# Performance work log

Hardware: AMD Instinct MI355X
Metric: run time of the kernel (lower is better)

Reference implementation:

```python
import jax, jax.numpy as jnp
import numpy as np

N, C_IN, C_OUT, T, V = 32, 4, 64, 6, 512


def setup_inputs() -> dict:
    key = jax.random.key(0)
    ks = jax.random.split(key, 8)
    x = jax.random.normal(ks[0], (N, C_IN, T, V), dtype=jnp.float32)
    # A carries 7 (unused) adjacency channels + 1 binary mask channel
    A = jax.random.randint(ks[1], (N, 8, V, V), 0, 2, dtype=jnp.int32)
    conv_w = jax.random.normal(ks[2], (C_OUT, C_IN), dtype=jnp.float32) / np.sqrt(C_IN).astype(np.float32)
    conv_b = jax.random.normal(ks[3], (C_OUT,), dtype=jnp.float32) * 0.02
    l2_w = jax.random.normal(ks[4], (1, T), dtype=jnp.float32) / np.sqrt(T).astype(np.float32)
    l2_b = jax.random.normal(ks[5], (1,), dtype=jnp.float32) * 0.02
    l1_w = jax.random.normal(ks[6], (1, 2 * C_OUT), dtype=jnp.float32) / np.sqrt(2 * C_OUT).astype(np.float32)
    l1_b = jax.random.normal(ks[7], (1,), dtype=jnp.float32) * 0.02
    return {"x": x, "A": A, "conv_w": conv_w, "conv_b": conv_b,
            "l2_w": l2_w, "l2_b": l2_b, "l1_w": l1_w, "l1_b": l1_b}


def reference(x, A, conv_w, conv_b, l2_w, l2_b, l1_w, l1_b):
    c = conv_w.shape[0]
    # 1x1 conv over (t, v): pure channel mix
    xc = jnp.einsum('nctv,oc->notv', x, conv_w) + conv_b[None, :, None, None]  # (n, 64, t, v)
    # temporal squeeze via l2: Linear(6 -> 1) on last (t) axis
    x1 = jnp.einsum('nctv,t->nvc', xc, l2_w[0]) + l2_b[0]  # (n, v, 64)
    # GAT-style pairwise score: l1(cat(x1_i, x1_j)) decomposes into two rank-1 terms
    e_i = x1 @ l1_w[0, :c]   # (n, v)
    e_j = x1 @ l1_w[0, c:]   # (n, v)
    scores = e_i[:, :, None] + e_j[:, None, :] + l1_b[0]  # (n, v, v), [n,i,j]
    scores = jnp.where(scores >= 0, scores, 0.2 * scores)  # LeakyReLU(0.2)
    # mask channel: A[:,7]; mask.long()==0 -> -inf
    mask = A[:, 7]  # (n, v, v) int
    scores = jnp.where(mask == 0, -jnp.inf, scores)
    p = jax.nn.softmax(scores, axis=2)
    p = jnp.where(jnp.isnan(p), 0.0, p)  # fully-masked rows -> 0
    # aggregate: nctv,ndvw->nctw with d=1
    out = jnp.einsum('nctv,nvw->nctw', xc, p)
    return out, p[:, None]  # (n, 64, t, v), (n, 1, v, v)
```

## Files before the change

### kernel.cpp

```cpp
#include <hip/hip_runtime.h>
#include <hip/hip_bf16.h>
#include <math.h>

#define NB   32
#define CIN  4
#define COUT 64
#define TT   6
#define VV   512
#define P_OFF (NB*COUT*TT*VV)
#define SPLITS 8
#define CH   (VV/SPLITS)
#define NROW 24
#define E_FLOATS (2*NB*VV)
#define PKW  516

typedef __attribute__((ext_vector_type(8))) short bf16x8;
typedef __attribute__((ext_vector_type(4))) float f32x4;

__device__ inline unsigned int pack2(float a, float b) {
    __hip_bfloat162 h = __float22bfloat162_rn(make_float2(a, b));
    return *reinterpret_cast<unsigned int*>(&h);
}

__global__ __launch_bounds__(256) void e_kernel(
    const float* __restrict__ x,
    const float* __restrict__ conv_w,
    const float* __restrict__ conv_b,
    const float* __restrict__ l2_w,
    const float* __restrict__ l2_b,
    const float* __restrict__ l1_w,
    float* __restrict__ e)
{
    __shared__ float W1[CIN], W2[CIN], cst[2];
    int tid = threadIdx.x;
    if (tid < CIN) {
        float w1 = 0.f, w2 = 0.f;
        for (int o = 0; o < COUT; ++o) {
            w1 += l1_w[o]        * conv_w[o*CIN + tid];
            w2 += l1_w[COUT + o] * conv_w[o*CIN + tid];
        }
        W1[tid] = w1; W2[tid] = w2;
    }
    if (tid == CIN) {
        float B1 = 0.f, B2 = 0.f, S1 = 0.f, S2 = 0.f;
        for (int o = 0; o < COUT; ++o) {
            B1 += l1_w[o]        * conv_b[o];
            B2 += l1_w[COUT + o] * conv_b[o];
            S1 += l1_w[o];
            S2 += l1_w[COUT + o];
        }
        float Ls = 0.f;
        for (int t = 0; t < TT; ++t) Ls += l2_w[t];
        cst[0] = Ls*B1 + l2_b[0]*S1;
        cst[1] = Ls*B2 + l2_b[0]*S2;
    }
    __syncthreads();

    int idx = blockIdx.x * 256 + tid;
    int n = idx >> 9, v = idx & (VV-1);
    float ei = cst[0], ej = cst[1];
    #pragma unroll
    for (int c = 0; c < CIN; ++c) {
        float wc1 = W1[c], wc2 = W2[c];
        #pragma unroll
        for (int t = 0; t < TT; ++t) {
            float xv = x[((n*CIN + c)*TT + t)*VV + v];
            float lw = l2_w[t];
            ei += lw*wc1*xv;
            ej += lw*wc2*xv;
        }
    }
    e[idx]         = ei;
    e[NB*VV + idx] = ej;
}

__global__ __launch_bounds__(512, 4) void fused_kernel(
    const float* __restrict__ x,
    const int*   __restrict__ A,
    const float* __restrict__ e,
    const float* __restrict__ l1_b,
    float*       __restrict__ p,
    float*       __restrict__ ypart)
{
    __shared__ float xst[CH][33];
    __shared__ unsigned int pk[16][PKW];

    int s = blockIdx.x;
    int n = blockIdx.y;
    int tid = threadIdx.x;
    int lane = tid & 63;
    int q = tid >> 6;

    for (int idx = tid; idx < CH*33; idx += 512) {
        int r = idx >> 6;
        int i = idx & 63;
        float v = 0.f;
        if (r < NROW)       v = x[((size_t)n*NROW + r)*VV + s*CH + i];
        else if (r == NROW) v = 1.f;
        xst[i][r] = v;
    }

    float l1b_val = l1_b[0];
    float4 ej0 = *(const float4*)(e + NB*VV + n*VV + lane*8);
    float4 ej1 = *(const float4*)(e + NB*VV + n*VV + lane*8 + 4);
    float ejv[8] = {ej0.x, ej0.y, ej0.z, ej0.w, ej1.x, ej1.y, ej1.z, ej1.w};

    const int* mbase = A + (size_t)(n*8 + 7)*VV*VV;

    f32x4 acc[2][4];
    #pragma unroll
    for (int mt = 0; mt < 2; ++mt)
        #pragma unroll
        for (int t = 0; t < 4; ++t) acc[mt][t] = (f32x4){0.f, 0.f, 0.f, 0.f};

    bf16x8 afr[2][2];

    int4 mA0, mA1, mB0, mB1;
    float bA, bB;
    {
        int i0 = s*CH + q*2;
        const int* mr = mbase + (size_t)i0*VV + lane*8;
        mA0 = *(const int4*)mr;       mA1 = *(const int4*)(mr + 4);
        mB0 = *(const int4*)(mr+VV);  mB1 = *(const int4*)(mr + VV + 4);
        bA = e[n*VV + i0]; bB = e[n*VV + i0 + 1];
    }

    for (int sub = 0; sub < 4; ++sub) {
        int i_gA = s*CH + sub*16 + q*2;

        int4 cA0 = mA0, cA1 = mA1, cB0 = mB0, cB1 = mB1;
        float biasA = bA + l1b_val, biasB = bB + l1b_val;

        if (sub < 3) {
            const int* mr = mbase + (size_t)(i_gA + 16)*VV + lane*8;
            mA0 = *(const int4*)mr;       mA1 = *(const int4*)(mr + 4);
            mB0 = *(const int4*)(mr+VV);  mB1 = *(const int4*)(mr + VV + 4);
            bA = e[n*VV + i_gA + 16]; bB = e[n*VV + i_gA + 17];
        }

        float svA[8], svB[8];
        int mkA[8] = {cA0.x,cA0.y,cA0.z,cA0.w, cA1.x,cA1.y,cA1.z,cA1.w};
        int mkB[8] = {cB0.x,cB0.y,cB0.z,cB0.w, cB1.x,cB1.y,cB1.z,cB1.w};
        #pragma unroll
        for (int m2 = 0; m2 < 8; ++m2) {
            float tA = biasA + ejv[m2]; tA = (tA >= 0.f) ? tA : 0.2f*tA;
            svA[m2] = (mkA[m2] == 0) ? -INFINITY : tA;
            float tB = biasB + ejv[m2]; tB = (tB >= 0.f) ? tB : 0.2f*tB;
            svB[m2] = (mkB[m2] == 0) ? -INFINITY : tB;
        }
        float mA = svA[0], mB = svB[0];
        #pragma unroll
        for (int m2 = 1; m2 < 8; ++m2) {
            mA = fmaxf(mA, svA[m2]); mB = fmaxf(mB, svB[m2]);
        }
        #pragma unroll
        for (int off = 32; off; off >>= 1) {
            mA = fmaxf(mA, __shfl_xor(mA, off));
            mB = fmaxf(mB, __shfl_xor(mB, off));
        }
        float sumA = 0.f, sumB = 0.f;
        if (mA > -INFINITY) {
            #pragma unroll
            for (int m2 = 0; m2 < 8; ++m2) { svA[m2] = __expf(svA[m2]-mA); sumA += svA[m2]; }
        } else {
            #pragma unroll
            for (int m2 = 0; m2 < 8; ++m2) svA[m2] = 0.f;
        }
        if (mB > -INFINITY) {
            #pragma unroll
            for (int m2 = 0; m2 < 8; ++m2) { svB[m2] = __expf(svB[m2]-mB); sumB += svB[m2]; }
        } else {
            #pragma unroll
            for (int m2 = 0; m2 < 8; ++m2) svB[m2] = 0.f;
        }
        #pragma unroll
        for (int off = 32; off; off >>= 1) {
            sumA += __shfl_xor(sumA, off);
            sumB += __shfl_xor(sumB, off);
        }
        float invA = (sumA > 0.f) ? 1.f/sumA : 0.f;
        float invB = (sumB > 0.f) ? 1.f/sumB : 0.f;
        #pragma unroll
        for (int m2 = 0; m2 < 8; ++m2) { svA[m2] *= invA; svB[m2] *= invB; }

        float* prA = p + ((size_t)(n*VV + i_gA))*VV + lane*8;
        float4 pA03 = {svA[0],svA[1],svA[2],svA[3]}, pA47 = {svA[4],svA[5],svA[6],svA[7]};
        float4 pB03 = {svB[0],svB[1],svB[2],svB[3]}, pB47 = {svB[4],svB[5],svB[6],svB[7]};
        *(float4*)prA            = pA03;
        *(float4*)(prA + 4)      = pA47;
        *(float4*)(prA + VV)     = pB03;
        *(float4*)(prA + VV + 4) = pB47;

        {
            int pr = (sub & 1)*8 + q;
            uint4 u0 = {pack2(svA[0],svB[0]), pack2(svA[1],svB[1]),
                        pack2(svA[2],svB[2]), pack2(svA[3],svB[3])};
            uint4 u1 = {pack2(svA[4],svB[4]), pack2(svA[5],svB[5]),
                        pack2(svA[6],svB[6]), pack2(svA[7],svB[7])};
            *(uint4*)&pk[pr][lane*8]     = u0;
            *(uint4*)&pk[pr][lane*8 + 4] = u1;
        }

        if (sub & 1) {
            __syncthreads();

            if (sub == 1) {
                #pragma unroll
                for (int g = 0; g < 2; ++g)
                    #pragma unroll
                    for (int mt = 0; mt < 2; ++mt) {
                        int r  = mt*16 + (lane & 15);
                        int kb = g*32 + (lane >> 4)*8;
                        union { unsigned int u[4]; bf16x8 v; } ua;
                        #pragma unroll
                        for (int t = 0; t < 4; ++t)
                            ua.u[t] = pack2(xst[kb + 2*t][r], xst[kb + 2*t + 1][r]);
                        afr[g][mt] = ua.v;
                    }
            }

            int g = sub >> 1;
            #pragma unroll
            for (int t = 0; t < 4; ++t) {
                int ncol = (q*4 + t)*16 + (lane & 15);
                union { unsigned int u[4]; bf16x8 v; } ub;
                #pragma unroll
                for (int jj = 0; jj < 4; ++jj)
                    ub.u[jj] = pk[(lane >> 4)*4 + jj][ncol];
                acc[0][t] = __builtin_amdgcn_mfma_f32_16x16x32_bf16(afr[g][0], ub.v, acc[0][t], 0, 0, 0);
                acc[1][t] = __builtin_amdgcn_mfma_f32_16x16x32_bf16(afr[g][1], ub.v, acc[1][t], 0, 0, 0);
            }
            if (sub == 1) __syncthreads();
        }
    }

    float* yo = ypart + (size_t)(s*NB + n)*25*VV;
    #pragma unroll
    for (int mt = 0; mt < 2; ++mt)
        #pragma unroll
        for (int t = 0; t < 4; ++t) {
            int ncol = (q*4 + t)*16 + (lane & 15);
            #pragma unroll
            for (int reg = 0; reg < 4; ++reg) {
                int row = mt*16 + (lane >> 4)*4 + reg;
                if (row < 25)
                    yo[(size_t)row*VV + ncol] = acc[mt][t][reg];
            }
        }
}

__global__ __launch_bounds__(256) void expand_kernel(
    const float* __restrict__ ypart,
    const float* __restrict__ conv_w,
    const float* __restrict__ conv_b,
    float*       __restrict__ out)
{
    __shared__ float ysm[25][64];
    __shared__ float wsm[COUT*CIN];
    __shared__ float bsm[COUT];

    int wc = blockIdx.x;
    int n  = blockIdx.y;
    int tid = threadIdx.x;

    if (tid < COUT*CIN) wsm[tid] = conv_w[tid];
    if (tid < COUT)     bsm[tid] = conv_b[tid];

    for (int l4 = tid; l4 < 400; l4 += 256) {
        int r = l4 >> 4, w4 = l4 & 15;
        float4 a = {0.f, 0.f, 0.f, 0.f};
        #pragma unroll
        for (int s = 0; s < SPLITS; ++s) {
            float4 v = *(const float4*)(ypart +
                ((size_t)(s*NB + n)*25 + r)*VV + wc*64 + w4*4);
            a.x += v.x; a.y += v.y; a.z += v.z; a.w += v.w;
        }
        *(float4*)&ysm[r][w4*4] = a;
    }
    __syncthreads();

    int w  = tid & 63;
    int og = tid >> 6;

    float y[25];
    #pragma unroll
    for (int r = 0; r < 25; ++r) y[r] = ysm[r][w];

    #pragma unroll
    for (int oo = 0; oo < 16; ++oo) {
        int o = og*16 + oo;
        float wb[CIN];
        #pragma unroll
        for (int c = 0; c < CIN; ++c) wb[c] = wsm[o*CIN + c];
        float bo = bsm[o];
        #pragma unroll
        for (int t = 0; t < TT; ++t) {
            float val = bo * y[24];
            #pragma unroll
            for (int c = 0; c < CIN; ++c) val = fmaf(wb[c], y[c*TT + t], val);
            out[((size_t)(n*COUT + o)*TT + t)*VV + wc*64 + w] = val;
        }
    }
}

extern "C" void kernel_launch(void* const* d_in, const int* in_sizes, int n_in,
                              void* d_out, int out_size, void* d_ws, size_t ws_size,
                              hipStream_t stream)
{
    const float* x      = (const float*)d_in[0];
    const int*   A      = (const int*)  d_in[1];
    const float* conv_w = (const float*)d_in[2];
    const float* conv_b = (const float*)d_in[3];
    const float* l2_w   = (const float*)d_in[4];
    const float* l2_b   = (const float*)d_in[5];
    const float* l1_w   = (const float*)d_in[6];
    const float* l1_b   = (const float*)d_in[7];

    float* out = (float*)d_out;
    float* pP  = out + P_OFF;
    float* e   = (float*)d_ws;
    float* yp  = e + E_FLOATS;

    e_kernel<<<NB*VV/256, 256, 0, stream>>>(x, conv_w, conv_b, l2_w, l2_b, l1_w, e);

    dim3 gf(SPLITS, NB);
    fused_kernel<<<gf, 512, 0, stream>>>(x, A, e, l1_b, pP, yp);

    dim3 ge(8, NB);
    expand_kernel<<<ge, 256, 0, stream>>>(yp, conv_w, conv_b, out);
}
```

Baseline: 34.62 us.

## Pre-pack mask channel into a bitmask in a wide prep kernel

A new prep pass, launched as thousands of extra blocks of the e-computation kernel, reads the int32 mask channel and packs it into one bit per entry in workspace. The fused softmax/aggregation kernel then stages its slice of the bitmask and the e_i values in shared memory instead of streaming int32 mask rows with register prefetch. The aim is to move the bandwidth-heavy mask read into a kernel with far more parallelism, away from the latency-bound fused kernel. The cost is an extra workspace write and read, plus one more __syncthreads in the fused kernel.

```diff
diff --git a/kernel.cpp b/kernel.cpp
--- a/kernel.cpp
+++ b/kernel.cpp
@@ -12,7 +12,9 @@
 #define CH   (VV/SPLITS)
 #define NROW 24
 #define E_FLOATS (2*NB*VV)
+#define BM_U32 (NB*VV*16)
 #define PKW  516
+#define MPK_BLOCKS 4096
 
 typedef __attribute__((ext_vector_type(8))) short bf16x8;
 typedef __attribute__((ext_vector_type(4))) float f32x4;
@@ -22,17 +24,38 @@
     return *reinterpret_cast<unsigned int*>(&h);
 }
 
-__global__ __launch_bounds__(256) void e_kernel(
+__global__ __launch_bounds__(256) void prep_kernel(
     const float* __restrict__ x,
+    const int*   __restrict__ A,
     const float* __restrict__ conv_w,
     const float* __restrict__ conv_b,
     const float* __restrict__ l2_w,
     const float* __restrict__ l2_b,
     const float* __restrict__ l1_w,
-    float* __restrict__ e)
+    float* __restrict__ e,
+    unsigned char* __restrict__ bm)
 {
     __shared__ float W1[CIN], W2[CIN], cst[2];
     int tid = threadIdx.x;
+    int b   = blockIdx.x;
+
+    if (b < MPK_BLOCKS) {
+        size_t t  = (size_t)b*256 + tid;
+        int nr    = (int)(t >> 6);
+        int byt   = (int)(t & 63);
+        int n     = nr >> 9, i = nr & 511;
+        const int* src = A + (((size_t)(n*8 + 7)*VV + i)*VV) + byt*8;
+        int4 a0 = *(const int4*)src;
+        int4 a1 = *(const int4*)(src + 4);
+        unsigned int byte =
+            (unsigned)(a0.x != 0)       | ((unsigned)(a0.y != 0) << 1) |
+            ((unsigned)(a0.z != 0) << 2) | ((unsigned)(a0.w != 0) << 3) |
+            ((unsigned)(a1.x != 0) << 4) | ((unsigned)(a1.y != 0) << 5) |
+            ((unsigned)(a1.z != 0) << 6) | ((unsigned)(a1.w != 0) << 7);
+        bm[(size_t)nr*64 + byt] = (unsigned char)byte;
+        return;
+    }
+
     if (tid < CIN) {
         float w1 = 0.f, w2 = 0.f;
         for (int o = 0; o < COUT; ++o) {
@@ -56,7 +79,7 @@
     }
     __syncthreads();
 
-    int idx = blockIdx.x * 256 + tid;
+    int idx = (b - MPK_BLOCKS) * 256 + tid;
     int n = idx >> 9, v = idx & (VV-1);
     float ei = cst[0], ej = cst[1];
     #pragma unroll
@@ -76,7 +99,7 @@
 
 __global__ __launch_bounds__(512, 4) void fused_kernel(
     const float* __restrict__ x,
-    const int*   __restrict__ A,
+    const unsigned int* __restrict__ bm32,
     const float* __restrict__ e,
     const float* __restrict__ l1_b,
     float*       __restrict__ p,
@@ -84,6 +107,8 @@
 {
     __shared__ float xst[CH][33];
     __shared__ unsigned int pk[16][PKW];
+    __shared__ unsigned int mlds[CH][16];
+    __shared__ float eld[CH];
 
     int s = blockIdx.x;
     int n = blockIdx.y;
@@ -99,14 +124,17 @@
         else if (r == NROW) v = 1.f;
         xst[i][r] = v;
     }
+    for (int l = tid; l < CH*16; l += 512) {
+        int il = l >> 4, d = l & 15;
+        mlds[il][d] = bm32[((size_t)n*VV + s*CH + il)*16 + d];
+    }
+    if (tid < CH) eld[tid] = e[n*VV + s*CH + tid];
 
     float l1b_val = l1_b[0];
     float4 ej0 = *(const float4*)(e + NB*VV + n*VV + lane*8);
     float4 ej1 = *(const float4*)(e + NB*VV + n*VV + lane*8 + 4);
     float ejv[8] = {ej0.x, ej0.y, ej0.z, ej0.w, ej1.x, ej1.y, ej1.z, ej1.w};
 
-    const int* mbase = A + (size_t)(n*8 + 7)*VV*VV;
-
     f32x4 acc[2][4];
     #pragma unroll
     for (int mt = 0; mt < 2; ++mt)
@@ -115,38 +143,24 @@
 
     bf16x8 afr[2][2];
 
-    int4 mA0, mA1, mB0, mB1;
-    float bA, bB;
-    {
-        int i0 = s*CH + q*2;
-        const int* mr = mbase + (size_t)i0*VV + lane*8;
-        mA0 = *(const int4*)mr;       mA1 = *(const int4*)(mr + 4);
-        mB0 = *(const int4*)(mr+VV);  mB1 = *(const int4*)(mr + VV + 4);
-        bA = e[n*VV + i0]; bB = e[n*VV + i0 + 1];
-    }
+    __syncthreads();
 
     for (int sub = 0; sub < 4; ++sub) {
-        int i_gA = s*CH + sub*16 + q*2;
-
-        int4 cA0 = mA0, cA1 = mA1, cB0 = mB0, cB1 = mB1;
-        float biasA = bA + l1b_val, biasB = bB + l1b_val;
-
-        if (sub < 3) {
-            const int* mr = mbase + (size_t)(i_gA + 16)*VV + lane*8;
-            mA0 = *(const int4*)mr;       mA1 = *(const int4*)(mr + 4);
-            mB0 = *(const int4*)(mr+VV);  mB1 = *(const int4*)(mr + VV + 4);
-            bA = e[n*VV + i_gA + 16]; bB = e[n*VV + i_gA + 17];
-        }
+        int ilA  = sub*16 + q*2;
+        int i_gA = s*CH + ilA;
+
+        unsigned int mbA = (mlds[ilA    ][lane >> 2] >> ((lane & 3)*8)) & 0xffu;
+        unsigned int mbB = (mlds[ilA + 1][lane >> 2] >> ((lane & 3)*8)) & 0xffu;
+        float biasA = eld[ilA]     + l1b_val;
+        float biasB = eld[ilA + 1] + l1b_val;
 
         float svA[8], svB[8];
-        int mkA[8] = {cA0.x,cA0.y,cA0.z,cA0.w, cA1.x,cA1.y,cA1.z,cA1.w};
-        int mkB[8] = {cB0.x,cB0.y,cB0.z,cB0.w, cB1.x,cB1.y,cB1.z,cB1.w};
         #pragma unroll
         for (int m2 = 0; m2 < 8; ++m2) {
             float tA = biasA + ejv[m2]; tA = (tA >= 0.f) ? tA : 0.2f*tA;
-            svA[m2] = (mkA[m2] == 0) ? -INFINITY : tA;
+            svA[m2] = ((mbA >> m2) & 1u) ? tA : -INFINITY;
             float tB = biasB + ejv[m2]; tB = (tB >= 0.f) ? tB : 0.2f*tB;
-            svB[m2] = (mkB[m2] == 0) ? -INFINITY : tB;
+            svB[m2] = ((mbB >> m2) & 1u) ? tB : -INFINITY;
         }
         float mA = svA[0], mB = svB[0];
         #pragma unroll
@@ -319,12 +333,14 @@
     float* out = (float*)d_out;
     float* pP  = out + P_OFF;
     float* e   = (float*)d_ws;
-    float* yp  = e + E_FLOATS;
-
-    e_kernel<<<NB*VV/256, 256, 0, stream>>>(x, conv_w, conv_b, l2_w, l2_b, l1_w, e);
+    unsigned int* bm = (unsigned int*)(e + E_FLOATS);
+    float* yp  = (float*)(bm + BM_U32);
+
+    prep_kernel<<<MPK_BLOCKS + NB*VV/256, 256, 0, stream>>>(
+        x, A, conv_w, conv_b, l2_w, l2_b, l1_w, e, (unsigned char*)bm);
 
     dim3 gf(SPLITS, NB);
-    fused_kernel<<<gf, 512, 0, stream>>>(x, A, e, l1_b, pP, yp);
+    fused_kernel<<<gf, 512, 0, stream>>>(x, bm, e, l1_b, pP, yp);
 
     dim3 ge(8, NB);
     expand_kernel<<<ge, 256, 0, stream>>>(yp, conv_w, conv_b, out);
```

Result: slower. 39.41 us (+13.9%).

## Fold score-vector kernel into fused attention kernel and widen expand grid

Applied to the files above, without the earlier changes.

Removes the separate e_kernel launch. Each fused block now recomputes the e_i/e_j projection vectors for its batch into shared memory, with l1_b folded into the e_j constant, and issues the first mask loads before that computation so their latency overlaps it. This saves a launch and a global round trip for e, at the cost of redundant per-block work across the 8 splits. The expand kernel also switches to 32-column tiles over a 16x32 grid, doubling block count to improve parallelism.

```diff
diff --git a/kernel.cpp b/kernel.cpp
--- a/kernel.cpp
+++ b/kernel.cpp
@@ -11,7 +11,6 @@
 #define SPLITS 8
 #define CH   (VV/SPLITS)
 #define NROW 24
-#define E_FLOATS (2*NB*VV)
 #define PKW  516
 
 typedef __attribute__((ext_vector_type(8))) short bf16x8;
@@ -22,25 +21,49 @@
     return *reinterpret_cast<unsigned int*>(&h);
 }
 
-__global__ __launch_bounds__(256) void e_kernel(
+__global__ __launch_bounds__(512, 4) void fused_kernel(
     const float* __restrict__ x,
+    const int*   __restrict__ A,
     const float* __restrict__ conv_w,
     const float* __restrict__ conv_b,
     const float* __restrict__ l2_w,
     const float* __restrict__ l2_b,
     const float* __restrict__ l1_w,
-    float* __restrict__ e)
+    const float* __restrict__ l1_b,
+    float*       __restrict__ p,
+    float*       __restrict__ ypart)
 {
-    __shared__ float W1[CIN], W2[CIN], cst[2];
+    __shared__ float xst[CH][33];
+    __shared__ unsigned int pk[16][PKW];
+    __shared__ float W1s[CIN], W2s[CIN], cst[2], l2s[TT];
+    __shared__ float ejl[VV];
+    __shared__ float eil[CH];
+
+    int s = blockIdx.x;
+    int n = blockIdx.y;
     int tid = threadIdx.x;
+    int lane = tid & 63;
+    int q = tid >> 6;
+
+    const int* mbase = A + (size_t)(n*8 + 7)*VV*VV;
+
+    int4 mA0, mA1, mB0, mB1;
+    {
+        int i0 = s*CH + q*2;
+        const int* mr = mbase + (size_t)i0*VV + lane*8;
+        mA0 = *(const int4*)mr;       mA1 = *(const int4*)(mr + 4);
+        mB0 = *(const int4*)(mr+VV);  mB1 = *(const int4*)(mr + VV + 4);
+    }
+
     if (tid < CIN) {
         float w1 = 0.f, w2 = 0.f;
         for (int o = 0; o < COUT; ++o) {
             w1 += l1_w[o]        * conv_w[o*CIN + tid];
             w2 += l1_w[COUT + o] * conv_w[o*CIN + tid];
         }
-        W1[tid] = w1; W2[tid] = w2;
-    }
+        W1s[tid] = w1; W2s[tid] = w2;
+    }
+    if (tid < TT) l2s[tid] = l2_w[tid];
     if (tid == CIN) {
         float B1 = 0.f, B2 = 0.f, S1 = 0.f, S2 = 0.f;
         for (int o = 0; o < COUT; ++o) {
@@ -52,44 +75,27 @@
         float Ls = 0.f;
         for (int t = 0; t < TT; ++t) Ls += l2_w[t];
         cst[0] = Ls*B1 + l2_b[0]*S1;
-        cst[1] = Ls*B2 + l2_b[0]*S2;
+        cst[1] = Ls*B2 + l2_b[0]*S2 + l1_b[0];
     }
     __syncthreads();
 
-    int idx = blockIdx.x * 256 + tid;
-    int n = idx >> 9, v = idx & (VV-1);
-    float ei = cst[0], ej = cst[1];
-    #pragma unroll
-    for (int c = 0; c < CIN; ++c) {
-        float wc1 = W1[c], wc2 = W2[c];
-        #pragma unroll
-        for (int t = 0; t < TT; ++t) {
-            float xv = x[((n*CIN + c)*TT + t)*VV + v];
-            float lw = l2_w[t];
-            ei += lw*wc1*xv;
-            ej += lw*wc2*xv;
-        }
-    }
-    e[idx]         = ei;
-    e[NB*VV + idx] = ej;
-}
-
-__global__ __launch_bounds__(512, 4) void fused_kernel(
-    const float* __restrict__ x,
-    const int*   __restrict__ A,
-    const float* __restrict__ e,
-    const float* __restrict__ l1_b,
-    float*       __restrict__ p,
-    float*       __restrict__ ypart)
-{
-    __shared__ float xst[CH][33];
-    __shared__ unsigned int pk[16][PKW];
-
-    int s = blockIdx.x;
-    int n = blockIdx.y;
-    int tid = threadIdx.x;
-    int lane = tid & 63;
-    int q = tid >> 6;
+    {
+        int j = tid;
+        float ei = cst[0], ej = cst[1];
+        #pragma unroll
+        for (int c = 0; c < CIN; ++c) {
+            float w1 = W1s[c], w2 = W2s[c];
+            #pragma unroll
+            for (int t = 0; t < TT; ++t) {
+                float lw = l2s[t];
+                float xv = x[((size_t)(n*CIN + c)*TT + t)*VV + j];
+                ei = fmaf(lw*w1, xv, ei);
+                ej = fmaf(lw*w2, xv, ej);
+            }
+        }
+        ejl[j] = ej;
+        if ((j >> 6) == s) eil[j & 63] = ei;
+    }
 
     for (int idx = tid; idx < CH*33; idx += 512) {
         int r = idx >> 6;
@@ -99,13 +105,11 @@
         else if (r == NROW) v = 1.f;
         xst[i][r] = v;
     }
-
-    float l1b_val = l1_b[0];
-    float4 ej0 = *(const float4*)(e + NB*VV + n*VV + lane*8);
-    float4 ej1 = *(const float4*)(e + NB*VV + n*VV + lane*8 + 4);
-    float ejv[8] = {ej0.x, ej0.y, ej0.z, ej0.w, ej1.x, ej1.y, ej1.z, ej1.w};
-
-    const int* mbase = A + (size_t)(n*8 + 7)*VV*VV;
+    __syncthreads();
+
+    float ejv[8];
+    #pragma unroll
+    for (int m = 0; m < 8; ++m) ejv[m] = ejl[lane*8 + m];
 
     f32x4 acc[2][4];
     #pragma unroll
@@ -115,27 +119,17 @@
 
     bf16x8 afr[2][2];
 
-    int4 mA0, mA1, mB0, mB1;
-    float bA, bB;
-    {
-        int i0 = s*CH + q*2;
-        const int* mr = mbase + (size_t)i0*VV + lane*8;
-        mA0 = *(const int4*)mr;       mA1 = *(const int4*)(mr + 4);
-        mB0 = *(const int4*)(mr+VV);  mB1 = *(const int4*)(mr + VV + 4);
-        bA = e[n*VV + i0]; bB = e[n*VV + i0 + 1];
-    }
-
     for (int sub = 0; sub < 4; ++sub) {
-        int i_gA = s*CH + sub*16 + q*2;
+        int ilA  = sub*16 + q*2;
+        int i_gA = s*CH + ilA;
 
         int4 cA0 = mA0, cA1 = mA1, cB0 = mB0, cB1 = mB1;
-        float biasA = bA + l1b_val, biasB = bB + l1b_val;
+        float biasA = eil[ilA], biasB = eil[ilA + 1];
 
         if (sub < 3) {
             const int* mr = mbase + (size_t)(i_gA + 16)*VV + lane*8;
             mA0 = *(const int4*)mr;       mA1 = *(const int4*)(mr + 4);
             mB0 = *(const int4*)(mr+VV);  mB1 = *(const int4*)(mr + VV + 4);
-            bA = e[n*VV + i_gA + 16]; bB = e[n*VV + i_gA + 17];
         }
 
         float svA[8], svB[8];
@@ -255,7 +249,7 @@
     const float* __restrict__ conv_b,
     float*       __restrict__ out)
 {
-    __shared__ float ysm[25][64];
+    __shared__ float ysm[25][32];
     __shared__ float wsm[COUT*CIN];
     __shared__ float bsm[COUT];
 
@@ -266,29 +260,29 @@
     if (tid < COUT*CIN) wsm[tid] = conv_w[tid];
     if (tid < COUT)     bsm[tid] = conv_b[tid];
 
-    for (int l4 = tid; l4 < 400; l4 += 256) {
-        int r = l4 >> 4, w4 = l4 & 15;
+    for (int l4 = tid; l4 < 200; l4 += 256) {
+        int r = l4 >> 3, w8 = l4 & 7;
         float4 a = {0.f, 0.f, 0.f, 0.f};
         #pragma unroll
         for (int s = 0; s < SPLITS; ++s) {
             float4 v = *(const float4*)(ypart +
-                ((size_t)(s*NB + n)*25 + r)*VV + wc*64 + w4*4);
+                ((size_t)(s*NB + n)*25 + r)*VV + wc*32 + w8*4);
             a.x += v.x; a.y += v.y; a.z += v.z; a.w += v.w;
         }
-        *(float4*)&ysm[r][w4*4] = a;
+        *(float4*)&ysm[r][w8*4] = a;
     }
     __syncthreads();
 
-    int w  = tid & 63;
-    int og = tid >> 6;
+    int w  = tid & 31;
+    int og = tid >> 5;
 
     float y[25];
     #pragma unroll
     for (int r = 0; r < 25; ++r) y[r] = ysm[r][w];
 
     #pragma unroll
-    for (int oo = 0; oo < 16; ++oo) {
-        int o = og*16 + oo;
+    for (int oo = 0; oo < 8; ++oo) {
+        int o = og*8 + oo;
         float wb[CIN];
         #pragma unroll
         for (int c = 0; c < CIN; ++c) wb[c] = wsm[o*CIN + c];
@@ -298,7 +292,7 @@
             float val = bo * y[24];
             #pragma unroll
             for (int c = 0; c < CIN; ++c) val = fmaf(wb[c], y[c*TT + t], val);
-            out[((size_t)(n*COUT + o)*TT + t)*VV + wc*64 + w] = val;
+            out[((size_t)(n*COUT + o)*TT + t)*VV + wc*32 + w] = val;
         }
     }
 }
@@ -318,14 +312,12 @@
 
     float* out = (float*)d_out;
     float* pP  = out + P_OFF;
-    float* e   = (float*)d_ws;
-    float* yp  = e + E_FLOATS;
-
-    e_kernel<<<NB*VV/256, 256, 0, stream>>>(x, conv_w, conv_b, l2_w, l2_b, l1_w, e);
+    float* yp  = (float*)d_ws;
 
     dim3 gf(SPLITS, NB);
-    fused_kernel<<<gf, 512, 0, stream>>>(x, A, e, l1_b, pP, yp);
-
-    dim3 ge(8, NB);
+    fused_kernel<<<gf, 512, 0, stream>>>(x, A, conv_w, conv_b, l2_w, l2_b,
+                                         l1_w, l1_b, pP, yp);
+
+    dim3 ge(16, NB);
     expand_kernel<<<ge, 256, 0, stream>>>(yp, conv_w, conv_b, out);
 }
```

Result: faster. 33.60 us, median of 2 (-2.9%).
